# Performance work log

Measured on AMD Instinct MI355X. Metric: run time of the kernel, lower is better.

Reference implementation:

```python
import jax, jax.numpy as jnp
import numpy as np

B, S, HID = 2, 2048, 2048
H, KV, D = 16, 8, 128          # query heads, kv heads, head dim
NREP = H // KV
EPS = 1e-6
THETA = 1000000.0
SCALE = 1.0 / np.sqrt(D)


def setup_inputs() -> dict:
    key = jax.random.key(0)
    ks = jax.random.split(key, 5)
    x = jax.random.normal(ks[0], (B, S, HID), jnp.float32)
    std = 0.02
    Wq = jax.random.normal(ks[1], (HID, H * D), jnp.float32) * std
    Wk = jax.random.normal(ks[2], (HID, KV * D), jnp.float32) * std
    Wv = jax.random.normal(ks[3], (HID, KV * D), jnp.float32) * std
    Wo = jax.random.normal(ks[4], (H * D, HID), jnp.float32) * std
    q_norm_w = jnp.ones((D,), jnp.float32)
    k_norm_w = jnp.ones((D,), jnp.float32)
    # standard RoPE cos/sin table: [S, D]
    inv_freq = 1.0 / (THETA ** (jnp.arange(0, D, 2, dtype=jnp.float32) / D))
    freqs = jnp.arange(S, dtype=jnp.float32)[:, None] * inv_freq[None, :]
    emb = jnp.concatenate([freqs, freqs], axis=-1)
    return {"x": x, "Wq": Wq, "Wk": Wk, "Wv": Wv, "Wo": Wo,
            "q_norm_w": q_norm_w, "k_norm_w": k_norm_w,
            "cos": jnp.cos(emb), "sin": jnp.sin(emb)}


def _rmsnorm(x, w, eps=EPS):
    var = jnp.mean(jnp.square(x), axis=-1, keepdims=True)
    return w * (x * jax.lax.rsqrt(var + eps))


def _rotate_half(x):
    x1, x2 = jnp.split(x, 2, axis=-1)
    return jnp.concatenate([-x2, x1], axis=-1)


def _rope(t, cos, sin):
    # t: [B, h, S, D]; cos/sin: [S, D]
    return t * cos[None, None] + _rotate_half(t) * sin[None, None]


def reference(x, Wq, Wk, Wv, Wo, q_norm_w, k_norm_w, cos, sin):
    q = (x @ Wq).reshape(B, S, H, D)
    k = (x @ Wk).reshape(B, S, KV, D)
    v = (x @ Wv).reshape(B, S, KV, D)
    q = _rmsnorm(q, q_norm_w).transpose(0, 2, 1, 3)   # [B, H, S, D]
    k = _rmsnorm(k, k_norm_w).transpose(0, 2, 1, 3)   # [B, KV, S, D]
    v = v.transpose(0, 2, 1, 3)                       # [B, KV, S, D]
    q = _rope(q, cos, sin)
    k = _rope(k, cos, sin)
    # GQA without materializing repeated K/V: group q heads per kv head
    qg = q.reshape(B, KV, NREP, S, D)
    scores = jnp.einsum('bgrsd,bgtd->bgrst', qg, k) * SCALE  # [B,KV,NREP,S,S]
    causal = jnp.tril(jnp.ones((S, S), dtype=bool))
    scores = jnp.where(causal, scores, jnp.finfo(scores.dtype).min)
    p = jax.nn.softmax(scores, axis=-1)
    out = jnp.einsum('bgrst,bgtd->bgrsd', p, v).reshape(B, H, S, D)
    out = out.transpose(0, 2, 1, 3).reshape(B, S, H * D)
    return out @ Wo
```

## Files before the change

### kernel.cpp

```cpp
#include <hip/hip_runtime.h>

typedef unsigned short u16;
typedef __bf16 bf16x8 __attribute__((ext_vector_type(8)));
typedef float f32x4 __attribute__((ext_vector_type(4)));

#define Bn 2
#define Sn 2048
#define HIDn 2048
#define Hn 16
#define KVn 8
#define Dn 128
#define SCALEf 0.08838834764831845f

__device__ __forceinline__ float b2f(u16 v) {
  return __builtin_bit_cast(float, (unsigned)v << 16);
}
__device__ __forceinline__ u16 f2b(float f) {
  unsigned u = __builtin_bit_cast(unsigned, f);
  u += 0x7fffu + ((u >> 16) & 1u);
  return (u16)(u >> 16);
}
__device__ __forceinline__ bool is_bf16(const void* det) {
  return *(const unsigned*)det == 0x3F803F80u;
}
__device__ __forceinline__ float ldx(const void* p, long i, bool isbf) {
  return isbf ? b2f(((const u16*)p)[i]) : ((const float*)p)[i];
}
__device__ __forceinline__ void gl_lds16(const u16* g, u16* l) {
  __builtin_amdgcn_global_load_lds(
      (unsigned int __attribute__((address_space(1)))*)g,
      (unsigned int __attribute__((address_space(3)))*)l, 16, 0, 0);
}

template <int CTRL>
__device__ __forceinline__ float dpp_mov(float x) {
  return __builtin_bit_cast(
      float, __builtin_amdgcn_update_dpp(0, __builtin_bit_cast(int, x), CTRL,
                                         0xF, 0xF, true));
}
__device__ __forceinline__ float red16_max(float x) {
  x = fmaxf(x, dpp_mov<0xB1>(x));
  x = fmaxf(x, dpp_mov<0x4E>(x));
  x = fmaxf(x, dpp_mov<0x141>(x));
  x = fmaxf(x, dpp_mov<0x140>(x));
  return x;
}
__device__ __forceinline__ float red16_sum(float x) {
  x += dpp_mov<0xB1>(x);
  x += dpp_mov<0x4E>(x);
  x += dpp_mov<0x141>(x);
  x += dpp_mov<0x140>(x);
  return x;
}

__global__ __launch_bounds__(256) void convert_x(
    const void* __restrict__ in, u16* __restrict__ out, const void* __restrict__ det) {
  bool isbf = is_bf16(det);
  long i = ((long)blockIdx.x * 256 + threadIdx.x) * 4;
  if (isbf) {
    *(ushort4*)(out + i) = *(const ushort4*)((const u16*)in + i);
  } else {
    float4 f = *(const float4*)((const float*)in + i);
    out[i] = f2b(f.x); out[i + 1] = f2b(f.y); out[i + 2] = f2b(f.z); out[i + 3] = f2b(f.w);
  }
}

__global__ __launch_bounds__(256) void transpose_any(
    const void* __restrict__ vin, u16* __restrict__ out, const void* __restrict__ det,
    int irs, int ors, long ib0, long ob0, int nb1, long ib1, long ob1) {
  __shared__ u16 tile[64][65];
  bool isbf = det ? is_bf16(det) : true;
  int bz = blockIdx.z;
  long ibase = (long)(bz / nb1) * ib0 + (long)(bz % nb1) * ib1;
  u16* op = out + (long)(bz / nb1) * ob0 + (long)(bz % nb1) * ob1;
  long r0 = (long)blockIdx.y * 64, c0 = (long)blockIdx.x * 64;
  int t = threadIdx.x;
  int tr = t >> 3, tc = (t & 7) * 8;
#pragma unroll
  for (int p = 0; p < 2; ++p) {
    int r = p * 32 + tr;
    long src = ibase + (r0 + r) * irs + c0 + tc;
    if (isbf) {
      const u16* ip = (const u16*)vin;
#pragma unroll
      for (int j = 0; j < 8; ++j) tile[r][tc + j] = ip[src + j];
    } else {
      const float* ip = (const float*)vin;
#pragma unroll
      for (int j = 0; j < 8; ++j) tile[r][tc + j] = f2b(ip[src + j]);
    }
  }
  __syncthreads();
#pragma unroll
  for (int p = 0; p < 2; ++p) {
    int r = p * 32 + tr;
    u16* dst = op + (c0 + r) * ors + r0 + tc;
#pragma unroll
    for (int j = 0; j < 8; ++j) dst[j] = tile[tc + j][r];
  }
}

__global__ __launch_bounds__(256) void gemm_bt(
    const u16* __restrict__ A, const u16* __restrict__ Bt, u16* __restrict__ C,
    float* __restrict__ Cf, const void* __restrict__ det, int N, int K) {
  __shared__ alignas(16) u16 As[128 * 32];
  __shared__ alignas(16) u16 Bs[128 * 32];
  int t = threadIdx.x;
  int wave = t >> 6, lane = t & 63, quad = lane >> 4, l15 = lane & 15;
  long bm = (long)blockIdx.y * 128, bn = (long)blockIdx.x * 128;
  int wm = (wave >> 1) * 64, wn = (wave & 1) * 64;
  f32x4 acc[4][4] = {};
  int sg = ((t & 3) ^ ((t >> 3) & 3)) * 8;
  const u16* Ab = A + (bm + (t >> 2)) * K + sg;
  const u16* Bb = Bt + (bn + (t >> 2)) * K + sg;
  int fg = (quad ^ ((l15 >> 1) & 3)) * 8;
  for (int k0 = 0; k0 < K; k0 += 32) {
    __syncthreads();
    gl_lds16(Ab + k0, As + t * 8);
    gl_lds16(Ab + (long)64 * K + k0, As + 2048 + t * 8);
    gl_lds16(Bb + k0, Bs + t * 8);
    gl_lds16(Bb + (long)64 * K + k0, Bs + 2048 + t * 8);
    __syncthreads();
    bf16x8 a[4], b[4];
#pragma unroll
    for (int i = 0; i < 4; ++i)
      a[i] = *(const bf16x8*)(As + (wm + i * 16 + l15) * 32 + fg);
#pragma unroll
    for (int j = 0; j < 4; ++j)
      b[j] = *(const bf16x8*)(Bs + (wn + j * 16 + l15) * 32 + fg);
#pragma unroll
    for (int i = 0; i < 4; ++i)
#pragma unroll
      for (int j = 0; j < 4; ++j)
        acc[i][j] = __builtin_amdgcn_mfma_f32_16x16x32_bf16(a[i], b[j], acc[i][j], 0, 0, 0);
  }
  bool tofloat = (Cf != nullptr) && !is_bf16(det);
#pragma unroll
  for (int i = 0; i < 4; ++i) {
    long row = bm + wm + i * 16 + quad * 4;
#pragma unroll
    for (int j = 0; j < 4; ++j) {
      long col = bn + wn + j * 16 + l15;
      if (tofloat) {
#pragma unroll
        for (int r = 0; r < 4; ++r) Cf[(row + r) * N + col] = acc[i][j][r];
      } else {
#pragma unroll
        for (int r = 0; r < 4; ++r) C[(row + r) * N + col] = f2b(acc[i][j][r]);
      }
    }
  }
}

__global__ __launch_bounds__(256) void gemm_proj_fused(
    const u16* __restrict__ A, const u16* __restrict__ Bt,
    u16* __restrict__ OutRope, u16* __restrict__ OutPlain, int nrope,
    const void* __restrict__ w, const void* __restrict__ cosb,
    const void* __restrict__ sinb, int K) {
  __shared__ alignas(16) u16 As[128 * 32];
  __shared__ alignas(16) u16 Bs[128 * 32];
  bool isbf = is_bf16(w);
  int t = threadIdx.x;
  int wave = t >> 6, lane = t & 63, quad = lane >> 4, l15 = lane & 15;
  long bm = (long)blockIdx.y * 128;
  int h = blockIdx.x;
  long bn = (long)h * 128;
  int wm = wave * 32;
  f32x4 acc[2][8] = {};
  int sg = ((t & 3) ^ ((t >> 3) & 3)) * 8;
  const u16* Ab = A + (bm + (t >> 2)) * K + sg;
  const u16* Bb = Bt + (bn + (t >> 2)) * K + sg;
  int fg = (quad ^ ((l15 >> 1) & 3)) * 8;
  for (int k0 = 0; k0 < K; k0 += 32) {
    __syncthreads();
    gl_lds16(Ab + k0, As + t * 8);
    gl_lds16(Ab + (long)64 * K + k0, As + 2048 + t * 8);
    gl_lds16(Bb + k0, Bs + t * 8);
    gl_lds16(Bb + (long)64 * K + k0, Bs + 2048 + t * 8);
    __syncthreads();
    bf16x8 a[2], b[8];
#pragma unroll
    for (int i = 0; i < 2; ++i)
      a[i] = *(const bf16x8*)(As + (wm + i * 16 + l15) * 32 + fg);
#pragma unroll
    for (int j = 0; j < 8; ++j)
      b[j] = *(const bf16x8*)(Bs + (j * 16 + l15) * 32 + fg);
#pragma unroll
    for (int i = 0; i < 2; ++i)
#pragma unroll
      for (int j = 0; j < 8; ++j)
        acc[i][j] = __builtin_amdgcn_mfma_f32_16x16x32_bf16(a[i], b[j], acc[i][j], 0, 0, 0);
  }
  if (h < nrope) {
#pragma unroll
    for (int i = 0; i < 2; ++i) {
#pragma unroll
      for (int r = 0; r < 4; ++r) {
        float ss = 0.f;
#pragma unroll
        for (int j = 0; j < 8; ++j) { float v = acc[i][j][r]; ss += v * v; }
        ss = red16_sum(ss);
        float scale = rsqrtf(ss * (1.0f / 128.0f) + 1e-6f);
        int m = (int)bm + wm + i * 16 + quad * 4 + r;
        int b = m >> 11, s = m & (Sn - 1);
        u16* dst = OutRope + (((long)b * nrope + h) * Sn + s) * Dn;
        long cb = (long)s * Dn;
#pragma unroll
        for (int j = 0; j < 4; ++j) {
          int c1i = j * 16 + l15, c2i = c1i + 64;
          float x1 = acc[i][j][r] * scale * ldx(w, c1i, isbf);
          float x2 = acc[i][j + 4][r] * scale * ldx(w, c2i, isbf);
          float c1 = ldx(cosb, cb + c1i, isbf), s1 = ldx(sinb, cb + c1i, isbf);
          float c2 = ldx(cosb, cb + c2i, isbf), s2 = ldx(sinb, cb + c2i, isbf);
          dst[c1i] = f2b(x1 * c1 - x2 * s1);
          dst[c2i] = f2b(x2 * c2 + x1 * s2);
        }
      }
    }
  } else {
    long col0 = (long)(h - nrope) * 128;
#pragma unroll
    for (int i = 0; i < 2; ++i) {
#pragma unroll
      for (int r = 0; r < 4; ++r) {
        long m = bm + wm + i * 16 + quad * 4 + r;
        u16* dst = OutPlain + m * 1024 + col0;
#pragma unroll
        for (int j = 0; j < 8; ++j) dst[j * 16 + l15] = f2b(acc[i][j][r]);
      }
    }
  }
}

__global__ __launch_bounds__(512) void attn_kernel(
    const u16* __restrict__ Qr, const u16* __restrict__ Kr,
    const u16* __restrict__ Vt, u16* __restrict__ Aout) {
  __shared__ alignas(16) u16 Ks[64 * 128];
  __shared__ alignas(16) u16 Vs[128 * 64];
  __shared__ alignas(16) u16 Ps[8][16 * 64];
  int t = threadIdx.x, wave = t >> 6, lane = t & 63, quad = lane >> 4, l15 = lane & 15;
  int bh = blockIdx.y, b = bh >> 4, h = bh & 15, kvh = h >> 1;
  const u16* kbase = Kr + ((long)b * KVn + kvh) * Sn * Dn;
  const u16* vbase = Vt + ((long)b * KVn + kvh) * (long)Dn * Sn;
  int krow = t >> 4;
  int kgr = ((t & 15) ^ (krow & 15)) * 8;
  int vrow = t >> 3;
  int vgr = ((t & 7) ^ (vrow & 7)) * 8;
  u16* ps = (u16*)Ps[wave];

  for (int half = 0; half < 2; ++half) {
    int qt = half == 0 ? (int)blockIdx.x : 15 - (int)blockIdx.x;
    int row0 = qt * 128 + wave * 16;
    const u16* qbase = Qr + (((long)b * Hn + h) * Sn + row0) * Dn;
    bf16x8 aq[4];
#pragma unroll
    for (int kt = 0; kt < 4; ++kt)
      aq[kt] = *(const bf16x8*)(qbase + l15 * Dn + kt * 32 + quad * 8);
    f32x4 o[8] = {};
    float mi[4], li[4];
#pragma unroll
    for (int r = 0; r < 4; ++r) { mi[r] = -1e30f; li[r] = 0.f; }
    int kv_end = qt * 128 + 128;
    for (int kv0 = 0; kv0 < kv_end; kv0 += 64) {
      __syncthreads();
      {
        const u16* kg = kbase + ((long)kv0 + krow) * Dn + kgr;
        gl_lds16(kg, Ks + t * 8);
        gl_lds16(kg + (long)32 * Dn, Ks + 4096 + t * 8);
        const u16* vg = vbase + (long)vrow * Sn + kv0 + vgr;
        gl_lds16(vg, Vs + t * 8);
        gl_lds16(vg + (long)64 * Sn, Vs + 4096 + t * 8);
      }
      __syncthreads();
      if (kv0 <= row0 + 15) {
        f32x4 sc[4] = {};
#pragma unroll
        for (int kt = 0; kt < 4; ++kt) {
          bf16x8 bk[4];
#pragma unroll
          for (int n = 0; n < 4; ++n)
            bk[n] = *(const bf16x8*)(Ks + (n * 16 + l15) * 128 + (((kt * 4 + quad) ^ l15) * 8));
#pragma unroll
          for (int n = 0; n < 4; ++n)
            sc[n] = __builtin_amdgcn_mfma_f32_16x16x32_bf16(aq[kt], bk[n], sc[n], 0, 0, 0);
        }
        f32x4 sv[4];
#pragma unroll
        for (int n = 0; n < 4; ++n)
#pragma unroll
          for (int r = 0; r < 4; ++r) sv[n][r] = sc[n][r] * SCALEf;
        if (kv0 + 63 > row0) {
#pragma unroll
          for (int n = 0; n < 4; ++n) {
            int col = kv0 + n * 16 + l15;
#pragma unroll
            for (int r = 0; r < 4; ++r)
              if (col > row0 + quad * 4 + r) sv[n][r] = -1e30f;
          }
        }
        float alpha[4], pr[4][4];
#pragma unroll
        for (int r = 0; r < 4; ++r) {
          float mx = fmaxf(fmaxf(sv[0][r], sv[1][r]), fmaxf(sv[2][r], sv[3][r]));
          mx = red16_max(mx);
          float mnew = fmaxf(mi[r], mx);
          alpha[r] = __expf(mi[r] - mnew);
          mi[r] = mnew;
          float rs = 0.f;
#pragma unroll
          for (int n = 0; n < 4; ++n) {
            float pv = __expf(sv[n][r] - mnew);
            pr[r][n] = pv;
            rs += pv;
          }
          rs = red16_sum(rs);
          li[r] = li[r] * alpha[r] + rs;
        }
#pragma unroll
        for (int n = 0; n < 8; ++n)
#pragma unroll
          for (int r = 0; r < 4; ++r) o[n][r] *= alpha[r];
#pragma unroll
        for (int n = 0; n < 4; ++n)
#pragma unroll
          for (int r = 0; r < 4; ++r) {
            int prow = quad * 4 + r;
            int pg = (n * 2 + (l15 >> 3)) ^ (prow & 7);
            ps[prow * 64 + pg * 8 + (l15 & 7)] = f2b(pr[r][n]);
          }
#pragma unroll
        for (int kt2 = 0; kt2 < 2; ++kt2) {
          bf16x8 ap = *(const bf16x8*)(ps + l15 * 64 + (((kt2 * 4 + quad) ^ (l15 & 7)) * 8));
#pragma unroll
          for (int n = 0; n < 8; ++n) {
            bf16x8 bv = *(const bf16x8*)(Vs + (n * 16 + l15) * 64 + (((kt2 * 4 + quad) ^ (l15 & 7)) * 8));
            o[n] = __builtin_amdgcn_mfma_f32_16x16x32_bf16(ap, bv, o[n], 0, 0, 0);
          }
        }
      }
    }
#pragma unroll
    for (int r = 0; r < 4; ++r) {
      long s = row0 + quad * 4 + r;
      float inv = 1.0f / li[r];
      u16* dst = Aout + (((long)b * Sn + s) * Hn + h) * Dn;
#pragma unroll
      for (int n = 0; n < 8; ++n) dst[n * 16 + l15] = f2b(o[n][r] * inv);
    }
  }
}

extern "C" void kernel_launch(void* const* d_in, const int* in_sizes, int n_in,
                              void* d_out, int out_size, void* d_ws, size_t ws_size,
                              hipStream_t stream) {
  (void)in_sizes; (void)n_in; (void)out_size; (void)ws_size;
  const void* x    = d_in[0];
  const void* Wq   = d_in[1];
  const void* Wk   = d_in[2];
  const void* Wv   = d_in[3];
  const void* Wo   = d_in[4];
  const void* qw   = d_in[5];
  const void* kw   = d_in[6];
  const void* cosb = d_in[7];
  const void* sinb = d_in[8];
  u16* ws = (u16*)d_ws;
  u16* dsc = (u16*)d_out;

  u16* Qr    = dsc + 0;
  u16* Kr    = dsc + 8388608;
  u16* Wslot = dsc + 12582912;
  u16* Vt    = dsc + 12582912;
  u16* xb   = ws + 0;
  u16* vb   = ws + 8388608;
  u16* attn = ws + 0;
  u16* WoT  = ws + 8388608;

  dim3 blk(256);
  convert_x<<<dim3(8192), blk, 0, stream>>>(x, xb, qw);
  transpose_any<<<dim3(32, 32, 1), blk, 0, stream>>>(Wq, Wslot, qw, 2048, 2048, 0, 0, 1, 0, 0);
  gemm_proj_fused<<<dim3(16, 32), blk, 0, stream>>>(xb, Wslot, Qr, nullptr, Hn, qw, cosb, sinb, 2048);
  transpose_any<<<dim3(16, 32, 1), blk, 0, stream>>>(Wk, Wslot, qw, 1024, 2048, 0, 0, 1, 0, 0);
  transpose_any<<<dim3(16, 32, 1), blk, 0, stream>>>(Wv, Wslot + (long)1024 * 2048, qw, 1024, 2048, 0, 0, 1, 0, 0);
  gemm_proj_fused<<<dim3(16, 32), blk, 0, stream>>>(xb, Wslot, Kr, vb, KVn, kw, cosb, sinb, 2048);
  transpose_any<<<dim3(2, 32, 16), blk, 0, stream>>>(
      vb, Vt, nullptr, KVn * Dn, Sn, 2097152L, 2097152L, KVn, (long)Dn, (long)Dn * Sn);
  attn_kernel<<<dim3(8, 32), dim3(512), 0, stream>>>(Qr, Kr, Vt, attn);
  transpose_any<<<dim3(32, 32, 1), blk, 0, stream>>>(Wo, WoT, qw, 2048, 2048, 0, 0, 1, 0, 0);
  gemm_bt<<<dim3(16, 32), blk, 0, stream>>>(attn, WoT, (u16*)d_out, (float*)d_out, qw, 2048, 2048);
}
```

Baseline: 414.0 us.

## Fuse QKV projections into one GEMM and register-prefetch attention K/V tiles

Merges the three weight transposes into a single prep kernel and the Q and KV projection GEMMs into one 32-column-block GEMM. That GEMM reads x directly and converts fp32 to bf16 while staging into LDS, so the separate convert pass goes away. The attention kernel now double-buffers K/V in LDS, prefetching the next tile through registers while computing the current one, and reuses the idle K buffer as the P scratch. The intent is to cut launches and extra passes over global memory and to hide load latency in attention. The cost is more register pressure and extra syncs, and the fp32 path loses the async global-to-LDS load.

Measured after the change: 473.1 us. 14.3% more time.

```diff
diff --git a/kernel.cpp b/kernel.cpp
--- a/kernel.cpp
+++ b/kernel.cpp
@@ -20,6 +20,9 @@
   u += 0x7fffu + ((u >> 16) & 1u);
   return (u16)(u >> 16);
 }
+__device__ __forceinline__ unsigned pack2(float lo, float hi) {
+  return (unsigned)f2b(lo) | ((unsigned)f2b(hi) << 16);
+}
 __device__ __forceinline__ bool is_bf16(const void* det) {
   return *(const unsigned*)det == 0x3F803F80u;
 }
@@ -53,15 +56,41 @@
   return x;
 }
 
-__global__ __launch_bounds__(256) void convert_x(
-    const void* __restrict__ in, u16* __restrict__ out, const void* __restrict__ det) {
+__global__ __launch_bounds__(256) void prep_weights(
+    const void* __restrict__ Wq, const void* __restrict__ Wk,
+    const void* __restrict__ Wv, u16* __restrict__ WT,
+    const void* __restrict__ det) {
+  __shared__ u16 tile[64][65];
   bool isbf = is_bf16(det);
-  long i = ((long)blockIdx.x * 256 + threadIdx.x) * 4;
-  if (isbf) {
-    *(ushort4*)(out + i) = *(const ushort4*)((const u16*)in + i);
-  } else {
-    float4 f = *(const float4*)((const float*)in + i);
-    out[i] = f2b(f.x); out[i + 1] = f2b(f.y); out[i + 2] = f2b(f.z); out[i + 3] = f2b(f.w);
+  int x = blockIdx.x;
+  const void* src;
+  int N, col0, drow0;
+  if (x < 32)      { src = Wq; N = 2048; col0 = x * 64;        drow0 = 0; }
+  else if (x < 48) { src = Wk; N = 1024; col0 = (x - 32) * 64; drow0 = 2048; }
+  else             { src = Wv; N = 1024; col0 = (x - 48) * 64; drow0 = 3072; }
+  long r0 = (long)blockIdx.y * 64;
+  int t = threadIdx.x, tr = t >> 3, tc = (t & 7) * 8;
+#pragma unroll
+  for (int p = 0; p < 2; ++p) {
+    int r = p * 32 + tr;
+    long s = (r0 + r) * N + col0 + tc;
+    if (isbf) {
+      const u16* ip = (const u16*)src;
+#pragma unroll
+      for (int j = 0; j < 8; ++j) tile[r][tc + j] = ip[s + j];
+    } else {
+      const float* ip = (const float*)src;
+#pragma unroll
+      for (int j = 0; j < 8; ++j) tile[r][tc + j] = f2b(ip[s + j]);
+    }
+  }
+  __syncthreads();
+#pragma unroll
+  for (int p = 0; p < 2; ++p) {
+    int r = p * 32 + tr;
+    u16* dst = WT + (long)(drow0 + col0 + r) * 2048 + r0 + tc;
+#pragma unroll
+    for (int j = 0; j < 8; ++j) dst[j] = tile[tc + j][r];
   }
 }
 
@@ -74,8 +103,7 @@
   long ibase = (long)(bz / nb1) * ib0 + (long)(bz % nb1) * ib1;
   u16* op = out + (long)(bz / nb1) * ob0 + (long)(bz % nb1) * ob1;
   long r0 = (long)blockIdx.y * 64, c0 = (long)blockIdx.x * 64;
-  int t = threadIdx.x;
-  int tr = t >> 3, tc = (t & 7) * 8;
+  int t = threadIdx.x, tr = t >> 3, tc = (t & 7) * 8;
 #pragma unroll
   for (int p = 0; p < 2; ++p) {
     int r = p * 32 + tr;
@@ -152,31 +180,45 @@
   }
 }
 
-__global__ __launch_bounds__(256) void gemm_proj_fused(
-    const u16* __restrict__ A, const u16* __restrict__ Bt,
-    u16* __restrict__ OutRope, u16* __restrict__ OutPlain, int nrope,
-    const void* __restrict__ w, const void* __restrict__ cosb,
-    const void* __restrict__ sinb, int K) {
+__global__ __launch_bounds__(256) void gemm_qkv(
+    const void* __restrict__ X, const u16* __restrict__ WT,
+    u16* __restrict__ Qr, u16* __restrict__ Kr, u16* __restrict__ Vb,
+    const void* __restrict__ qw, const void* __restrict__ kw,
+    const void* __restrict__ cosb, const void* __restrict__ sinb) {
   __shared__ alignas(16) u16 As[128 * 32];
   __shared__ alignas(16) u16 Bs[128 * 32];
-  bool isbf = is_bf16(w);
+  const int K = 2048;
+  bool isbf = is_bf16(qw);
   int t = threadIdx.x;
   int wave = t >> 6, lane = t & 63, quad = lane >> 4, l15 = lane & 15;
   long bm = (long)blockIdx.y * 128;
   int h = blockIdx.x;
-  long bn = (long)h * 128;
   int wm = wave * 32;
   f32x4 acc[2][8] = {};
   int sg = ((t & 3) ^ ((t >> 3) & 3)) * 8;
-  const u16* Ab = A + (bm + (t >> 2)) * K + sg;
-  const u16* Bb = Bt + (bn + (t >> 2)) * K + sg;
+  long a0 = (bm + (t >> 2)) * (long)K + sg;
+  long a1 = a0 + (long)64 * K;
+  const u16* Bb = WT + ((long)h * 128 + (t >> 2)) * K + sg;
   int fg = (quad ^ ((l15 >> 1) & 3)) * 8;
+  const float* xf = (const float*)X;
+  const u16* xh = (const u16*)X;
   for (int k0 = 0; k0 < K; k0 += 32) {
     __syncthreads();
-    gl_lds16(Ab + k0, As + t * 8);
-    gl_lds16(Ab + (long)64 * K + k0, As + 2048 + t * 8);
     gl_lds16(Bb + k0, Bs + t * 8);
     gl_lds16(Bb + (long)64 * K + k0, Bs + 2048 + t * 8);
+    if (isbf) {
+      gl_lds16(xh + a0 + k0, As + t * 8);
+      gl_lds16(xh + a1 + k0, As + 2048 + t * 8);
+    } else {
+      float4 f0 = *(const float4*)(xf + a0 + k0);
+      float4 f1 = *(const float4*)(xf + a0 + k0 + 4);
+      float4 f2 = *(const float4*)(xf + a1 + k0);
+      float4 f3 = *(const float4*)(xf + a1 + k0 + 4);
+      uint4 w0 = {pack2(f0.x, f0.y), pack2(f0.z, f0.w), pack2(f1.x, f1.y), pack2(f1.z, f1.w)};
+      uint4 w1 = {pack2(f2.x, f2.y), pack2(f2.z, f2.w), pack2(f3.x, f3.y), pack2(f3.z, f3.w)};
+      *(uint4*)(As + t * 8) = w0;
+      *(uint4*)(As + 2048 + t * 8) = w1;
+    }
     __syncthreads();
     bf16x8 a[2], b[8];
 #pragma unroll
@@ -191,7 +233,11 @@
       for (int j = 0; j < 8; ++j)
         acc[i][j] = __builtin_amdgcn_mfma_f32_16x16x32_bf16(a[i], b[j], acc[i][j], 0, 0, 0);
   }
-  if (h < nrope) {
+  if (h < 24) {
+    const void* w = (h < Hn) ? qw : kw;
+    int nh = (h < Hn) ? Hn : KVn;
+    int hh = (h < Hn) ? h : h - Hn;
+    u16* OutR = (h < Hn) ? Qr : Kr;
 #pragma unroll
     for (int i = 0; i < 2; ++i) {
 #pragma unroll
@@ -203,7 +249,7 @@
         float scale = rsqrtf(ss * (1.0f / 128.0f) + 1e-6f);
         int m = (int)bm + wm + i * 16 + quad * 4 + r;
         int b = m >> 11, s = m & (Sn - 1);
-        u16* dst = OutRope + (((long)b * nrope + h) * Sn + s) * Dn;
+        u16* dst = OutR + (((long)b * nh + hh) * Sn + s) * Dn;
         long cb = (long)s * Dn;
 #pragma unroll
         for (int j = 0; j < 4; ++j) {
@@ -218,13 +264,13 @@
       }
     }
   } else {
-    long col0 = (long)(h - nrope) * 128;
+    long col0 = (long)(h - 24) * 128;
 #pragma unroll
     for (int i = 0; i < 2; ++i) {
 #pragma unroll
       for (int r = 0; r < 4; ++r) {
         long m = bm + wm + i * 16 + quad * 4 + r;
-        u16* dst = OutPlain + m * 1024 + col0;
+        u16* dst = Vb + m * 1024 + col0;
 #pragma unroll
         for (int j = 0; j < 8; ++j) dst[j * 16 + l15] = f2b(acc[i][j][r]);
       }
@@ -235,9 +281,8 @@
 __global__ __launch_bounds__(512) void attn_kernel(
     const u16* __restrict__ Qr, const u16* __restrict__ Kr,
     const u16* __restrict__ Vt, u16* __restrict__ Aout) {
-  __shared__ alignas(16) u16 Ks[64 * 128];
-  __shared__ alignas(16) u16 Vs[128 * 64];
-  __shared__ alignas(16) u16 Ps[8][16 * 64];
+  __shared__ alignas(16) u16 Ks[2][64 * 128];
+  __shared__ alignas(16) u16 Vs[2][128 * 64];
   int t = threadIdx.x, wave = t >> 6, lane = t & 63, quad = lane >> 4, l15 = lane & 15;
   int bh = blockIdx.y, b = bh >> 4, h = bh & 15, kvh = h >> 1;
   const u16* kbase = Kr + ((long)b * KVn + kvh) * Sn * Dn;
@@ -246,7 +291,8 @@
   int kgr = ((t & 15) ^ (krow & 15)) * 8;
   int vrow = t >> 3;
   int vgr = ((t & 7) ^ (vrow & 7)) * 8;
-  u16* ps = (u16*)Ps[wave];
+  const u16* kg0 = kbase + (long)krow * Dn + kgr;
+  const u16* vg0 = vbase + (long)vrow * Sn + vgr;
 
   for (int half = 0; half < 2; ++half) {
     int qt = half == 0 ? (int)blockIdx.x : 15 - (int)blockIdx.x;
@@ -260,26 +306,37 @@
     float mi[4], li[4];
 #pragma unroll
     for (int r = 0; r < 4; ++r) { mi[r] = -1e30f; li[r] = 0.f; }
-    int kv_end = qt * 128 + 128;
-    for (int kv0 = 0; kv0 < kv_end; kv0 += 64) {
+    int nIter = qt * 2 + 2;
+    uint4 ka = *(const uint4*)(kg0);
+    uint4 kb2 = *(const uint4*)(kg0 + (long)32 * Dn);
+    uint4 va = *(const uint4*)(vg0);
+    uint4 vb2 = *(const uint4*)(vg0 + (long)64 * Sn);
+    for (int it = 0; it < nIter; ++it) {
+      int bufc = it & 1, bufn = bufc ^ 1;
+      *(uint4*)(Ks[bufc] + t * 8) = ka;
+      *(uint4*)(Ks[bufc] + 4096 + t * 8) = kb2;
+      *(uint4*)(Vs[bufc] + t * 8) = va;
+      *(uint4*)(Vs[bufc] + 4096 + t * 8) = vb2;
       __syncthreads();
-      {
-        const u16* kg = kbase + ((long)kv0 + krow) * Dn + kgr;
-        gl_lds16(kg, Ks + t * 8);
-        gl_lds16(kg + (long)32 * Dn, Ks + 4096 + t * 8);
-        const u16* vg = vbase + (long)vrow * Sn + kv0 + vgr;
-        gl_lds16(vg, Vs + t * 8);
-        gl_lds16(vg + (long)64 * Sn, Vs + 4096 + t * 8);
+      if (it + 1 < nIter) {
+        long off = (long)(it + 1) * 64;
+        ka = *(const uint4*)(kg0 + off * Dn);
+        kb2 = *(const uint4*)(kg0 + off * Dn + (long)32 * Dn);
+        va = *(const uint4*)(vg0 + off);
+        vb2 = *(const uint4*)(vg0 + off + (long)64 * Sn);
       }
-      __syncthreads();
+      int kv0 = it * 64;
       if (kv0 <= row0 + 15) {
+        const u16* ksb = Ks[bufc];
+        const u16* vsb = Vs[bufc];
+        u16* ps = Ks[bufn] + wave * 1024;
         f32x4 sc[4] = {};
 #pragma unroll
         for (int kt = 0; kt < 4; ++kt) {
           bf16x8 bk[4];
 #pragma unroll
           for (int n = 0; n < 4; ++n)
-            bk[n] = *(const bf16x8*)(Ks + (n * 16 + l15) * 128 + (((kt * 4 + quad) ^ l15) * 8));
+            bk[n] = *(const bf16x8*)(ksb + (n * 16 + l15) * 128 + (((kt * 4 + quad) ^ l15) * 8));
 #pragma unroll
           for (int n = 0; n < 4; ++n)
             sc[n] = __builtin_amdgcn_mfma_f32_16x16x32_bf16(aq[kt], bk[n], sc[n], 0, 0, 0);
@@ -333,11 +390,12 @@
           bf16x8 ap = *(const bf16x8*)(ps + l15 * 64 + (((kt2 * 4 + quad) ^ (l15 & 7)) * 8));
 #pragma unroll
           for (int n = 0; n < 8; ++n) {
-            bf16x8 bv = *(const bf16x8*)(Vs + (n * 16 + l15) * 64 + (((kt2 * 4 + quad) ^ (l15 & 7)) * 8));
+            bf16x8 bv = *(const bf16x8*)(vsb + (n * 16 + l15) * 64 + (((kt2 * 4 + quad) ^ (l15 & 7)) * 8));
             o[n] = __builtin_amdgcn_mfma_f32_16x16x32_bf16(ap, bv, o[n], 0, 0, 0);
           }
         }
       }
+      __syncthreads();
     }
 #pragma unroll
     for (int r = 0; r < 4; ++r) {
@@ -347,6 +405,7 @@
 #pragma unroll
       for (int n = 0; n < 8; ++n) dst[n * 16 + l15] = f2b(o[n][r] * inv);
     }
+    __syncthreads();
   }
 }
 
@@ -366,22 +425,17 @@
   u16* ws = (u16*)d_ws;
   u16* dsc = (u16*)d_out;
 
-  u16* Qr    = dsc + 0;
-  u16* Kr    = dsc + 8388608;
-  u16* Wslot = dsc + 12582912;
-  u16* Vt    = dsc + 12582912;
-  u16* xb   = ws + 0;
+  u16* Qr = dsc + 0;
+  u16* Kr = dsc + 8388608;
+  u16* Vt = dsc + 12582912;
+  u16* WT   = ws + 0;
   u16* vb   = ws + 8388608;
   u16* attn = ws + 0;
   u16* WoT  = ws + 8388608;
 
   dim3 blk(256);
-  convert_x<<<dim3(8192), blk, 0, stream>>>(x, xb, qw);
-  transpose_any<<<dim3(32, 32, 1), blk, 0, stream>>>(Wq, Wslot, qw, 2048, 2048, 0, 0, 1, 0, 0);
-  gemm_proj_fused<<<dim3(16, 32), blk, 0, stream>>>(xb, Wslot, Qr, nullptr, Hn, qw, cosb, sinb, 2048);
-  transpose_any<<<dim3(16, 32, 1), blk, 0, stream>>>(Wk, Wslot, qw, 1024, 2048, 0, 0, 1, 0, 0);
-  transpose_any<<<dim3(16, 32, 1), blk, 0, stream>>>(Wv, Wslot + (long)1024 * 2048, qw, 1024, 2048, 0, 0, 1, 0, 0);
-  gemm_proj_fused<<<dim3(16, 32), blk, 0, stream>>>(xb, Wslot, Kr, vb, KVn, kw, cosb, sinb, 2048);
+  prep_weights<<<dim3(64, 32), blk, 0, stream>>>(Wq, Wk, Wv, WT, qw);
+  gemm_qkv<<<dim3(32, 32), blk, 0, stream>>>(x, WT, Qr, Kr, vb, qw, kw, cosb, sinb);
   transpose_any<<<dim3(2, 32, 16), blk, 0, stream>>>(
       vb, Vt, nullptr, KVn * Dn, Sn, 2097152L, 2097152L, KVn, (long)Dn, (long)Dn * Sn);
   attn_kernel<<<dim3(8, 32), dim3(512), 0, stream>>>(Qr, Kr, Vt, attn);
```
